# Kernel optimization log

Measured on AMD Instinct MI355X. Metric: run time of the kernel, lower is better.

## Reference

```python
import jax, jax.numpy as jnp
import numpy as np

N_LIG, N_PROT, K = 1024, 8192, 48
N = N_LIG + N_PROT
HID, FEAT, DEPTH = 256, 32, 5
NF = 6                      # sinusoid frequencies -> 12-dim distance embedding
EDGE_DIM = 4 * NF           # per-block dist emb (12) + top-level dist emb (12)
NORM = 5.0                  # agg_norm_factor
_FREQS = (2.0 * np.pi * 4.0 ** np.arange(NF) / 15.0).astype(np.float32)

def sin_emb(d2):
    # d2: [E,1] squared distances -> [E, 2*NF] sinusoidal embedding
    d = jnp.sqrt(d2 + 1e-8)
    x = d * _FREQS
    return jnp.concatenate([jnp.sin(x), jnp.cos(x)], axis=-1)

def knn_edges(coors):
    # KNN (k=48, no self loops) restricted to ligand query nodes (first N_LIG),
    # matching edges[:, :N_lig*k] slicing of knn_graph(flow='target_to_source').
    c = jax.lax.stop_gradient(coors)
    lig = c[:N_LIG]
    d2 = jnp.sum((lig[:, None, :] - c[None, :, :]) ** 2, axis=-1)  # [N_LIG, N]
    d2 = d2.at[jnp.arange(N_LIG), jnp.arange(N_LIG)].set(jnp.inf)
    _, idx = jax.lax.top_k(-d2, K)                                  # [N_LIG, K]
    row = jnp.repeat(jnp.arange(N_LIG), K)
    col = idx.reshape(-1)
    return row, col

def egnn(h, x, row, col, W_in, b_in, W_out, b_out, edge_W1, edge_b1, edge_W2, edge_b2, att_W, att_b, node_W1, node_b1, node_W2, node_b2, coord_W1, coord_b1, coord_W2, coord_b2, coord_W3):
    # EDM-style EGNN: per block 1 GCL (edge MLP + attention gate + node MLP residual)
    # followed by an equivariant coordinate update; sin distance embedding.
    emb0 = sin_emb(jnp.sum((x[row] - x[col]) ** 2, axis=-1, keepdims=True))
    h = h @ W_in + b_in
    for l in range(DEPTH):
        diff = x[row] - x[col]                         # [E,3]
        d2 = jnp.sum(diff ** 2, axis=-1, keepdims=True)
        cdiff = diff / (jnp.sqrt(d2 + 1e-8) + 1.0)     # norm_constant = 1
        ea = jnp.concatenate([sin_emb(d2), emb0], axis=-1)  # [E, EDGE_DIM]
        m = jax.nn.silu(jnp.concatenate([h[row], h[col], ea], axis=-1) @ edge_W1[l] + edge_b1[l])
        m = jax.nn.silu(m @ edge_W2[l] + edge_b2[l])
        m = m * jax.nn.sigmoid(m @ att_W[l] + att_b[l])         # attention gate
        agg = jax.ops.segment_sum(m, row, num_segments=N) / NORM
        u = jax.nn.silu(jnp.concatenate([h, agg], axis=-1) @ node_W1[l] + node_b1[l])
        h = h + (u @ node_W2[l] + node_b2[l])                    # residual node update
        c = jax.nn.silu(jnp.concatenate([h[row], h[col], ea], axis=-1) @ coord_W1[l] + coord_b1[l])  # use_latest_h
        c = jax.nn.silu(c @ coord_W2[l] + coord_b2[l])
        x = x + jax.ops.segment_sum(cdiff * (c @ coord_W3[l]), row, num_segments=N) / NORM
    return h @ W_out + b_out, x

def setup_inputs():
    key = jax.random.key(0)
    ks = jax.random.split(key, 24)
    f32 = jnp.float32
    def nrm(i, shape, scale=0.05):
        return jax.random.normal(ks[i], shape, dtype=f32) * scale
    return {
        'protein_positions': nrm(0, (N_PROT, 3), 3.0),
        'protein_ele': jax.random.randint(ks[1], (N_PROT,), 0, 5),
        'protein_amino_acid': jax.random.randint(ks[2], (N_PROT,), 0, 20),
        'protein_is_backbone': jax.random.randint(ks[3], (N_PROT,), 0, 2),
        'Xt_pos': nrm(4, (N_LIG, 3), 1.0),
        'Xt_features': nrm(5, (N_LIG, FEAT), 1.0),
        't': jax.random.randint(ks[6], (N_LIG,), 0, 1000),
        'Wt_time': nrm(7, (1000, 8), 1.0),
        'W_ele': nrm(8, (5, 16), 1.0),
        'W_aa': nrm(9, (20, 16), 1.0),
        'W_bb': nrm(10, (2, 8), 1.0),
        'W_in': nrm(11, (40, HID)), 'b_in': jnp.zeros((HID,), f32),
        'W_out': nrm(12, (HID, FEAT)), 'b_out': jnp.zeros((FEAT,), f32),
        'edge_W1': nrm(13, (DEPTH, 2 * HID + EDGE_DIM, HID)), 'edge_b1': jnp.zeros((DEPTH, HID), f32),
        'edge_W2': nrm(14, (DEPTH, HID, HID)), 'edge_b2': jnp.zeros((DEPTH, HID), f32),
        'att_W': nrm(15, (DEPTH, HID, 1)), 'att_b': jnp.zeros((DEPTH, 1), f32),
        'node_W1': nrm(16, (DEPTH, 2 * HID, HID)), 'node_b1': jnp.zeros((DEPTH, HID), f32),
        'node_W2': nrm(17, (DEPTH, HID, HID)), 'node_b2': jnp.zeros((DEPTH, HID), f32),
        'coord_W1': nrm(18, (DEPTH, 2 * HID + EDGE_DIM, HID)), 'coord_b1': jnp.zeros((DEPTH, HID), f32),
        'coord_W2': nrm(19, (DEPTH, HID, HID)), 'coord_b2': jnp.zeros((DEPTH, HID), f32),
        'coord_W3': nrm(20, (DEPTH, HID, 1), 0.001),
        'pos_w': jnp.ones((1, 1), f32),
    }

def reference(protein_positions, protein_ele, protein_amino_acid, protein_is_backbone, Xt_pos, Xt_features, t, Wt_time, W_ele, W_aa, W_bb, W_in, b_in, W_out, b_out, edge_W1, edge_b1, edge_W2, edge_b2, att_W, att_b, node_W1, node_b1, node_W2, node_b2, coord_W1, coord_b1, coord_W2, coord_b2, coord_W3, pos_w):
    prot_feat = jnp.concatenate([W_ele[protein_ele], W_aa[protein_amino_acid], W_bb[protein_is_backbone]], axis=-1)  # [N_PROT,40]
    feats = jnp.concatenate([jnp.concatenate([Xt_features, Wt_time[t]], axis=-1), prot_feat], axis=0)  # [N,40]
    coors = jnp.concatenate([Xt_pos, protein_positions], axis=0)  # [N,3]
    row, col = knn_edges(coors)
    h, x = egnn(feats, coors, row, col, W_in, b_in, W_out, b_out, edge_W1, edge_b1, edge_W2, edge_b2, att_W, att_b, node_W1, node_b1, node_W2, node_b2, coord_W1, coord_b1, coord_W2, coord_b2, coord_W3)
    # pos_linear: Linear(1,1,bias=False) applied elementwise == scalar multiply
    return x[:N_LIG] * pos_w[0, 0], h[:N_LIG]
```

## Files before the change

kernel.cpp:

```cpp
#include <hip/hip_runtime.h>
#include <hip/hip_bf16.h>
#include <math.h>

#define N_LIGC 1024
#define NTOT 9216
#define KNN 48
#define HID 256
#define DEPTHC 5
#define ETOT (N_LIGC*KNN)
#define KBINS 4096
#define PACK_BLKS 1484

typedef unsigned short u16;
typedef __attribute__((ext_vector_type(8))) short bf16x8;
typedef __attribute__((ext_vector_type(4))) float f32x4;

__device__ __forceinline__ float freq_f(int i){
  double p = (double)(1 << (2*i));
  return (float)((2.0*3.14159265358979323846)*p/15.0);
}
__device__ __forceinline__ float silu_f(float v){
  return v*__builtin_amdgcn_rcpf(1.0f+__expf(-v));
}
__device__ __forceinline__ float sigm_f(float v){
  return __builtin_amdgcn_rcpf(1.0f+__expf(-v));
}
__device__ __forceinline__ u16 f2b(float f){
  unsigned int u = __float_as_uint(f);
  return (u16)((u + 0x7fffu + ((u>>16)&1u)) >> 16);
}
__device__ __forceinline__ float b2f(u16 u){
  union { unsigned int i; float f; } c; c.i = ((unsigned int)u)<<16; return c.f;
}
__device__ __forceinline__ u16 f2b_p(float f){
  union { __hip_bfloat16 h; u16 u; } c; c.h = __float2bfloat16(f); return c.u;
}

__device__ __forceinline__ void pack_one(const float* __restrict__ src,
    u16* __restrict__ dst, int srcK, int kOff, int Keff, int Kp, int N, int idx)
{
  int lane = idx & 63;
  int rest = idx >> 6;
  int Nt = N >> 4;
  int n0 = rest % Nt;
  int rest2 = rest / Nt;
  int Kt = Kp >> 5;
  int k0 = rest2 % Kt;
  int layer = rest2 / Kt;
  int kq = lane >> 4, nl = lane & 15;
  int kb = k0*32 + kq*8, n = n0*16 + nl;
  u16 o[8];
  #pragma unroll
  for (int j=0;j<8;j++){
    int k = kb + j;
    float v = (k < Keff) ? src[((size_t)layer*srcK + kOff + k)*N + n] : 0.f;
    o[j] = f2b_p(v);
  }
  *(uint4*)(dst + (size_t)idx*8) = *(uint4*)o;
}

__global__ __launch_bounds__(256) void k_prep(
    const float* eW1, const float* eW2, const float* nW1, const float* nW2,
    const float* cW1, const float* cW2, const float* Wout,
    u16* eW1abP, u16* eW1cP, u16* eW2p, u16* nW1p, u16* nW2p,
    u16* cW1abP, u16* cW1cP, u16* cW2p, u16* WoutP,
    const float* __restrict__ protPos, const int* __restrict__ protEle,
    const int* __restrict__ protAA, const int* __restrict__ protBB,
    const float* __restrict__ XtPos, const float* __restrict__ XtFeat,
    const int* __restrict__ tArr, const float* __restrict__ WtTime,
    const float* __restrict__ Wele, const float* __restrict__ Waa,
    const float* __restrict__ Wbb,
    const float* __restrict__ Win, const float* __restrict__ bin,
    float* __restrict__ X0, float* __restrict__ X1,
    float* __restrict__ h, u16* __restrict__ h_bf)
{
  __shared__ float sF[8*40];
  if (blockIdx.x < PACK_BLKS){
    int idx = blockIdx.x*256 + threadIdx.x;
    if (idx < 81920){ pack_one(eW1, eW1abP, 536, 0,   512, 512, 256, idx); return; } idx -= 81920;
    if (idx < 5120 ){ pack_one(eW1, eW1cP,  536, 512, 24,  32,  256, idx); return; } idx -= 5120;
    if (idx < 40960){ pack_one(eW2, eW2p,   256, 0,   256, 256, 256, idx); return; } idx -= 40960;
    if (idx < 81920){ pack_one(nW1, nW1p,   512, 0,   512, 512, 256, idx); return; } idx -= 81920;
    if (idx < 40960){ pack_one(nW2, nW2p,   256, 0,   256, 256, 256, idx); return; } idx -= 40960;
    if (idx < 81920){ pack_one(cW1, cW1abP, 536, 0,   512, 512, 256, idx); return; } idx -= 81920;
    if (idx < 5120 ){ pack_one(cW1, cW1cP,  536, 512, 24,  32,  256, idx); return; } idx -= 5120;
    if (idx < 40960){ pack_one(cW2, cW2p,   256, 0,   256, 256, 256, idx); return; } idx -= 40960;
    if (idx < 1024 ){ pack_one(Wout, WoutP, 256, 0,   256, 256, 32,  idx); return; }
    return;
  }
  int blk=blockIdx.x - PACK_BLKS, tid=threadIdx.x;
  int n0=blk*8;
  for (int x=tid; x<344; x+=256){
    if (x < 320){
      int n = x/40, k = x%40;
      int node = n0+n;
      float v;
      if (node < N_LIGC){
        if (k < 32) v = XtFeat[node*32+k];
        else        v = WtTime[tArr[node]*8 + (k-32)];
      } else {
        int p = node - N_LIGC;
        if (k < 16)      v = Wele[protEle[p]*16 + k];
        else if (k < 32) v = Waa[protAA[p]*16 + (k-16)];
        else             v = Wbb[protBB[p]*8 + (k-32)];
      }
      sF[n*40+k] = v;
    } else {
      int r = x-320; int n = r/3, c = r%3;
      int node = n0+n;
      float v = (node < N_LIGC) ? XtPos[node*3+c] : protPos[(node-N_LIGC)*3+c];
      X0[node*3+c] = v; X1[node*3+c] = v;
    }
  }
  __syncthreads();
  float acc[8];
  float b=bin[tid];
  #pragma unroll
  for (int n=0;n<8;n++) acc[n]=b;
  for (int k=0;k<40;k++){
    float w=Win[k*HID+tid];
    #pragma unroll
    for (int n=0;n<8;n++) acc[n]+=sF[n*40+k]*w;
  }
  #pragma unroll
  for (int n=0;n<8;n++){
    h[(size_t)(n0+n)*HID+tid]=acc[n];
    h_bf[(size_t)(n0+n)*HID+tid]=f2b_p(acc[n]);
  }
}

__global__ __launch_bounds__(256) void k_knn(const float* __restrict__ X,
    int* __restrict__ col, u16* __restrict__ emb0)
{
  __shared__ unsigned int hist[KBINS];
  __shared__ unsigned int part[256];
  __shared__ float selD[KNN];
  __shared__ int   candI[512];
  __shared__ float candV[512];
  __shared__ int sB, sCless, sNeed, sNsel, sNcand;
  int b = blockIdx.x, tid = threadIdx.x;
  for (int i=tid;i<KBINS;i+=256) hist[i]=0u;
  if (tid==0){ sNsel=0; sNcand=0; }
  float px = X[b*3+0], py = X[b*3+1], pz = X[b*3+2];
  __syncthreads();
  #pragma unroll 4
  for (int j=0;j<36;j++){
    int i = tid + 256*j;
    float dx = __fsub_rn(px, X[i*3+0]);
    float dy = __fsub_rn(py, X[i*3+1]);
    float dz = __fsub_rn(pz, X[i*3+2]);
    float d2 = __fadd_rn(__fadd_rn(__fmul_rn(dx,dx),__fmul_rn(dy,dy)),__fmul_rn(dz,dz));
    if (i==b) d2 = INFINITY;
    unsigned key = __float_as_uint(d2) >> 19;
    atomicAdd(&hist[key], 1u);
  }
  __syncthreads();
  {
    unsigned s=0;
    #pragma unroll 4
    for (int k=0;k<16;k++) s += hist[tid*16+k];
    part[tid]=s;
  }
  __syncthreads();
  if (tid==0){
    unsigned c=0; int chunk=0;
    for (int t=0;t<256;t++){
      if (c + part[t] >= (unsigned)KNN){ chunk=t; break; }
      c += part[t];
    }
    int bin = chunk*16;
    for (;;bin++){
      unsigned hh = hist[bin];
      if (c + hh >= (unsigned)KNN) break;
      c += hh;
    }
    sB = bin; sCless = (int)c; sNeed = KNN - (int)c;
  }
  __syncthreads();
  int B = sB;
  #pragma unroll 4
  for (int j=0;j<36;j++){
    int i = tid + 256*j;
    float dx = __fsub_rn(px, X[i*3+0]);
    float dy = __fsub_rn(py, X[i*3+1]);
    float dz = __fsub_rn(pz, X[i*3+2]);
    float d2 = __fadd_rn(__fadd_rn(__fmul_rn(dx,dx),__fmul_rn(dy,dy)),__fmul_rn(dz,dz));
    if (i==b) d2 = INFINITY;
    int key = (int)(__float_as_uint(d2) >> 19);
    if (key < B){
      int p = atomicAdd(&sNsel, 1);
      col[b*KNN+p] = i; selD[p] = d2;
    } else if (key == B){
      int c = atomicAdd(&sNcand, 1);
      if (c < 512){ candI[c] = i; candV[c] = d2; }
    }
  }
  __syncthreads();
  if (tid < 64){
    int m = sNcand; if (m > 512) m = 512;
    int need = sNeed, base = sCless;
    float cv[8]; int ci[8];
    #pragma unroll
    for (int k=0;k<8;k++){
      int c = tid + 64*k;
      if (c < m){ ci[k]=candI[c]; cv[k]=candV[c]; }
      else      { ci[k]=0x7fffffff; cv[k]=INFINITY; }
    }
    for (int it=0; it<need; it++){
      float bv=INFINITY; int bi=0x7fffffff; int bk=0;
      #pragma unroll
      for (int k=0;k<8;k++){
        if (cv[k]<bv || (cv[k]==bv && ci[k]<bi)){ bv=cv[k]; bi=ci[k]; bk=k; }
      }
      int bslot = tid + 64*bk;
      #pragma unroll
      for (int off=32; off>=1; off>>=1){
        float ov = __shfl_down(bv, off);
        int   oi = __shfl_down(bi, off);
        int   os = __shfl_down(bslot, off);
        if (ov < bv || (ov==bv && oi<bi)){ bv=ov; bi=oi; bslot=os; }
      }
      int wslot = __shfl(bslot, 0);
      if (tid==0){ col[b*KNN+base+it]=bi; selD[base+it]=bv; }
      if ((wslot & 63) == tid) cv[wslot >> 6] = INFINITY;
    }
  }
  __syncthreads();
  if (tid < KNN){
    float d = sqrtf(selD[tid] + 1e-8f);
    int base = (b*KNN+tid)*12;
    #pragma unroll
    for (int i=0;i<6;i++){
      float fr = freq_f(i);
      emb0[base+i]   = f2b_p(sinf(d*fr));
      emb0[base+6+i] = f2b_p(cosf(d*fr));
    }
  }
}

__global__ __launch_bounds__(256) void k_pq(const u16* __restrict__ h_bf,
    const u16* __restrict__ Wab, float* __restrict__ R, u16* __restrict__ Qb, int l)
{
  __shared__ __align__(16) u16 sA[32*264];
  int blk=blockIdx.x, tid=threadIdx.x;
  int lane=tid&63, ng=tid>>6, quad=lane>>4, nl=lane&15;
  for (int t=tid; t<32*32; t+=256){
    int i=t>>5, q=t&31;
    uint4 v = ((const uint4*)(h_bf + (size_t)(blk*32+i)*HID))[q];
    *(uint4*)(sA + i*264 + q*8) = v;
  }
  __syncthreads();
  const u16* Wl = Wab + (size_t)l*512*HID;
  f32x4 zero4 = {0.f,0.f,0.f,0.f};
  f32x4 aQ[2][4];
  #pragma unroll
  for (int i=0;i<2;i++){ aQ[i][0]=zero4; aQ[i][1]=zero4; aQ[i][2]=zero4; aQ[i][3]=zero4; }
  #pragma unroll 2
  for (int k0=0;k0<8;k0++){
    bf16x8 a0 = *(const bf16x8*)(sA + (0*16+nl)*264 + k0*32 + quad*8);
    bf16x8 a1 = *(const bf16x8*)(sA + (1*16+nl)*264 + k0*32 + quad*8);
    const u16* wb = Wl + ((size_t)((k0+8)*16 + ng*4)*64 + lane)*8;
    bf16x8 b0 = *(const bf16x8*)(wb);
    bf16x8 b1 = *(const bf16x8*)(wb + 512);
    bf16x8 b2 = *(const bf16x8*)(wb + 1024);
    bf16x8 b3 = *(const bf16x8*)(wb + 1536);
    aQ[0][0]=__builtin_amdgcn_mfma_f32_16x16x32_bf16(a0,b0,aQ[0][0],0,0,0);
    aQ[0][1]=__builtin_amdgcn_mfma_f32_16x16x32_bf16(a0,b1,aQ[0][1],0,0,0);
    aQ[0][2]=__builtin_amdgcn_mfma_f32_16x16x32_bf16(a0,b2,aQ[0][2],0,0,0);
    aQ[0][3]=__builtin_amdgcn_mfma_f32_16x16x32_bf16(a0,b3,aQ[0][3],0,0,0);
    aQ[1][0]=__builtin_amdgcn_mfma_f32_16x16x32_bf16(a1,b0,aQ[1][0],0,0,0);
    aQ[1][1]=__builtin_amdgcn_mfma_f32_16x16x32_bf16(a1,b1,aQ[1][1],0,0,0);
    aQ[1][2]=__builtin_amdgcn_mfma_f32_16x16x32_bf16(a1,b2,aQ[1][2],0,0,0);
    aQ[1][3]=__builtin_amdgcn_mfma_f32_16x16x32_bf16(a1,b3,aQ[1][3],0,0,0);
  }
  #pragma unroll
  for (int mt=0;mt<2;mt++)
  #pragma unroll
  for (int nt=0;nt<4;nt++){
    int n = ng*64 + nt*16 + nl;
    #pragma unroll
    for (int r=0;r<4;r++){
      int node = blk*32 + mt*16 + quad*4 + r;
      Qb[(size_t)node*HID + n] = f2b(aQ[mt][nt][r]);
    }
  }
  if (blk < 32){
    f32x4 aR[2][4];
    #pragma unroll
    for (int i=0;i<2;i++){ aR[i][0]=zero4; aR[i][1]=zero4; aR[i][2]=zero4; aR[i][3]=zero4; }
    #pragma unroll 2
    for (int k0=0;k0<8;k0++){
      bf16x8 a0 = *(const bf16x8*)(sA + (0*16+nl)*264 + k0*32 + quad*8);
      bf16x8 a1 = *(const bf16x8*)(sA + (1*16+nl)*264 + k0*32 + quad*8);
      const u16* wb = Wl + ((size_t)(k0*16 + ng*4)*64 + lane)*8;
      bf16x8 b0 = *(const bf16x8*)(wb);
      bf16x8 b1 = *(const bf16x8*)(wb + 512);
      bf16x8 b2 = *(const bf16x8*)(wb + 1024);
      bf16x8 b3 = *(const bf16x8*)(wb + 1536);
      aR[0][0]=__builtin_amdgcn_mfma_f32_16x16x32_bf16(a0,b0,aR[0][0],0,0,0);
      aR[0][1]=__builtin_amdgcn_mfma_f32_16x16x32_bf16(a0,b1,aR[0][1],0,0,0);
      aR[0][2]=__builtin_amdgcn_mfma_f32_16x16x32_bf16(a0,b2,aR[0][2],0,0,0);
      aR[0][3]=__builtin_amdgcn_mfma_f32_16x16x32_bf16(a0,b3,aR[0][3],0,0,0);
      aR[1][0]=__builtin_amdgcn_mfma_f32_16x16x32_bf16(a1,b0,aR[1][0],0,0,0);
      aR[1][1]=__builtin_amdgcn_mfma_f32_16x16x32_bf16(a1,b1,aR[1][1],0,0,0);
      aR[1][2]=__builtin_amdgcn_mfma_f32_16x16x32_bf16(a1,b2,aR[1][2],0,0,0);
      aR[1][3]=__builtin_amdgcn_mfma_f32_16x16x32_bf16(a1,b3,aR[1][3],0,0,0);
    }
    #pragma unroll
    for (int mt=0;mt<2;mt++)
    #pragma unroll
    for (int nt=0;nt<4;nt++){
      int n = ng*64 + nt*16 + nl;
      #pragma unroll
      for (int r=0;r<4;r++){
        int node = blk*32 + mt*16 + quad*4 + r;
        R[(size_t)node*HID + n] = aR[mt][nt][r];
      }
    }
  }
}

__global__ __launch_bounds__(256,4) void k_comb_edge(
    const u16* __restrict__ Qb, const float* __restrict__ R,
    const float* __restrict__ xc,
    const int* __restrict__ colIdx, const u16* __restrict__ emb0,
    const u16* __restrict__ W1cP, const float* __restrict__ B1,
    const u16* __restrict__ W2p, const float* __restrict__ B2,
    const float* __restrict__ attW, const float* __restrict__ attB,
    u16* __restrict__ agg_bf, int l)
{
  __shared__ __align__(16) u16 sQ[48*264];
  __shared__ __align__(16) u16 sEA[48*40];
  __shared__ float sR[256];
  __shared__ int sCol[48];
  __shared__ float sD[48];
  __shared__ float sSig[48];
  __shared__ float sDot[48][4];

  int row = blockIdx.x, tid = threadIdx.x;
  int lane = tid & 63, ng = tid >> 6;
  int quad = lane >> 4, nl = lane & 15;

  if (tid < 48) sCol[tid] = colIdx[(size_t)row*KNN + tid];
  sR[tid] = R[(size_t)row*HID + tid];
  __syncthreads();
  for (int t = tid; t < 48*32; t += 256){
    int e = t >> 5, q = t & 31;
    uint4 v = ((const uint4*)(Qb + (size_t)sCol[e]*HID))[q];
    *(uint4*)(sQ + e*264 + q*8) = v;
  }
  if (tid < 48){
    int cg = sCol[tid];
    float dx = xc[row*3+0]-xc[cg*3+0];
    float dy = xc[row*3+1]-xc[cg*3+1];
    float dz = xc[row*3+2]-xc[cg*3+2];
    float d = sqrtf(dx*dx+dy*dy+dz*dz + 1e-8f);
    sD[tid] = d;
    const unsigned int* ep = (const unsigned int*)(emb0 + ((size_t)row*KNN + tid)*12);
    unsigned int* dd = (unsigned int*)(sEA + tid*40 + 12);
    #pragma unroll
    for (int i=0;i<6;i++) dd[i] = ep[i];
    u16* ea = sEA + tid*40;
    #pragma unroll
    for (int i=24;i<32;i++) ea[i] = 0;
  }
  __syncthreads();
  for (int t=tid; t<288; t+=256){
    int e = t/6, i = t - 6*e;
    float fr = 0.41887903f * (float)(1 << (2*i));
    float x = sD[e]*fr;
    u16* ea = sEA + e*40;
    ea[i]   = f2b(__sinf(x));
    ea[6+i] = f2b(__cosf(x));
  }
  __syncthreads();

  f32x4 zero4 = {0.f,0.f,0.f,0.f};
  f32x4 acc[3][4];
  #pragma unroll
  for (int i=0;i<3;i++){ acc[i][0]=zero4; acc[i][1]=zero4; acc[i][2]=zero4; acc[i][3]=zero4; }
  {
    const u16* Wc = W1cP + (size_t)l*32*HID;
    const u16* wb = Wc + ((size_t)(ng*4)*64 + lane)*8;
    bf16x8 b0 = *(const bf16x8*)(wb);
    bf16x8 b1 = *(const bf16x8*)(wb + 512);
    bf16x8 b2 = *(const bf16x8*)(wb + 1024);
    bf16x8 b3 = *(const bf16x8*)(wb + 1536);
    bf16x8 a0 = *(const bf16x8*)(sEA + (0*16+nl)*40 + quad*8);
    bf16x8 a1 = *(const bf16x8*)(sEA + (1*16+nl)*40 + quad*8);
    bf16x8 a2 = *(const bf16x8*)(sEA + (2*16+nl)*40 + quad*8);
    acc[0][0]=__builtin_amdgcn_mfma_f32_16x16x32_bf16(a0,b0,acc[0][0],0,0,0);
    acc[0][1]=__builtin_amdgcn_mfma_f32_16x16x32_bf16(a0,b1,acc[0][1],0,0,0);
    acc[0][2]=__builtin_amdgcn_mfma_f32_16x16x32_bf16(a0,b2,acc[0][2],0,0,0);
    acc[0][3]=__builtin_amdgcn_mfma_f32_16x16x32_bf16(a0,b3,acc[0][3],0,0,0);
    acc[1][0]=__builtin_amdgcn_mfma_f32_16x16x32_bf16(a1,b0,acc[1][0],0,0,0);
    acc[1][1]=__builtin_amdgcn_mfma_f32_16x16x32_bf16(a1,b1,acc[1][1],0,0,0);
    acc[1][2]=__builtin_amdgcn_mfma_f32_16x16x32_bf16(a1,b2,acc[1][2],0,0,0);
    acc[1][3]=__builtin_amdgcn_mfma_f32_16x16x32_bf16(a1,b3,acc[1][3],0,0,0);
    acc[2][0]=__builtin_amdgcn_mfma_f32_16x16x32_bf16(a2,b0,acc[2][0],0,0,0);
    acc[2][1]=__builtin_amdgcn_mfma_f32_16x16x32_bf16(a2,b1,acc[2][1],0,0,0);
    acc[2][2]=__builtin_amdgcn_mfma_f32_16x16x32_bf16(a2,b2,acc[2][2],0,0,0);
    acc[2][3]=__builtin_amdgcn_mfma_f32_16x16x32_bf16(a2,b3,acc[2][3],0,0,0);
  }
  #pragma unroll
  for (int mt=0;mt<3;mt++)
  #pragma unroll
  for (int nt=0;nt<4;nt++){
    int n = ng*64 + nt*16 + nl;
    float bb = B1[l*HID + n] + sR[n];
    #pragma unroll
    for (int r=0;r<4;r++){
      int m = mt*16 + quad*4 + r;
      float v = acc[mt][nt][r] + bb + b2f(sQ[m*264 + n]);
      sQ[m*264 + n] = f2b(silu_f(v));
    }
  }
  __syncthreads();

  f32x4 acc2[3][4];
  #pragma unroll
  for (int i=0;i<3;i++){ acc2[i][0]=zero4; acc2[i][1]=zero4; acc2[i][2]=zero4; acc2[i][3]=zero4; }
  const u16* W2 = W2p + (size_t)l*HID*HID;
  #pragma unroll 2
  for (int k0=0;k0<8;k0++){
    bf16x8 a0 = *(const bf16x8*)(sQ + (0*16+nl)*264 + k0*32 + quad*8);
    bf16x8 a1 = *(const bf16x8*)(sQ + (1*16+nl)*264 + k0*32 + quad*8);
    bf16x8 a2 = *(const bf16x8*)(sQ + (2*16+nl)*264 + k0*32 + quad*8);
    const u16* wb = W2 + ((size_t)(k0*16 + ng*4)*64 + lane)*8;
    bf16x8 b0 = *(const bf16x8*)(wb);
    bf16x8 b1 = *(const bf16x8*)(wb + 512);
    bf16x8 b2 = *(const bf16x8*)(wb + 1024);
    bf16x8 b3 = *(const bf16x8*)(wb + 1536);
    acc2[0][0]=__builtin_amdgcn_mfma_f32_16x16x32_bf16(a0,b0,acc2[0][0],0,0,0);
    acc2[0][1]=__builtin_amdgcn_mfma_f32_16x16x32_bf16(a0,b1,acc2[0][1],0,0,0);
    acc2[0][2]=__builtin_amdgcn_mfma_f32_16x16x32_bf16(a0,b2,acc2[0][2],0,0,0);
    acc2[0][3]=__builtin_amdgcn_mfma_f32_16x16x32_bf16(a0,b3,acc2[0][3],0,0,0);
    acc2[1][0]=__builtin_amdgcn_mfma_f32_16x16x32_bf16(a1,b0,acc2[1][0],0,0,0);
    acc2[1][1]=__builtin_amdgcn_mfma_f32_16x16x32_bf16(a1,b1,acc2[1][1],0,0,0);
    acc2[1][2]=__builtin_amdgcn_mfma_f32_16x16x32_bf16(a1,b2,acc2[1][2],0,0,0);
    acc2[1][3]=__builtin_amdgcn_mfma_f32_16x16x32_bf16(a1,b3,acc2[1][3],0,0,0);
    acc2[2][0]=__builtin_amdgcn_mfma_f32_16x16x32_bf16(a2,b0,acc2[2][0],0,0,0);
    acc2[2][1]=__builtin_amdgcn_mfma_f32_16x16x32_bf16(a2,b1,acc2[2][1],0,0,0);
    acc2[2][2]=__builtin_amdgcn_mfma_f32_16x16x32_bf16(a2,b2,acc2[2][2],0,0,0);
    acc2[2][3]=__builtin_amdgcn_mfma_f32_16x16x32_bf16(a2,b3,acc2[2][3],0,0,0);
  }
  float aw[4], bb2[4];
  #pragma unroll
  for (int nt=0;nt<4;nt++){
    int n = ng*64 + nt*16 + nl;
    aw[nt]  = attW[l*HID + n];
    bb2[nt] = B2[l*HID + n];
  }
  float dotp[3][4];
  #pragma unroll
  for (int mt=0;mt<3;mt++){
    #pragma unroll
    for (int r=0;r<4;r++) dotp[mt][r] = 0.f;
    #pragma unroll
    for (int nt=0;nt<4;nt++){
      #pragma unroll
      for (int r=0;r<4;r++){
        float s = silu_f(acc2[mt][nt][r] + bb2[nt]);
        acc2[mt][nt][r] = s;
        dotp[mt][r] += s*aw[nt];
      }
    }
  }
  #pragma unroll
  for (int off=1; off<16; off<<=1){
    #pragma unroll
    for (int mt=0;mt<3;mt++)
    #pragma unroll
    for (int r=0;r<4;r++)
      dotp[mt][r] += __shfl_xor(dotp[mt][r], off);
  }
  if (nl == 0){
    #pragma unroll
    for (int mt=0;mt<3;mt++)
    #pragma unroll
    for (int r=0;r<4;r++)
      sDot[mt*16 + quad*4 + r][ng] = dotp[mt][r];
  }
  __syncthreads();
  if (tid < 48) sSig[tid] = sigm_f(sDot[tid][0]+sDot[tid][1]+sDot[tid][2]+sDot[tid][3] + attB[l]);
  __syncthreads();
  float sgv[3][4];
  #pragma unroll
  for (int mt=0;mt<3;mt++)
  #pragma unroll
  for (int r=0;r<4;r++)
    sgv[mt][r] = sSig[mt*16 + quad*4 + r];
  #pragma unroll
  for (int nt=0;nt<4;nt++){
    float a = 0.f;
    #pragma unroll
    for (int mt=0;mt<3;mt++)
    #pragma unroll
    for (int r=0;r<4;r++)
      a += acc2[mt][nt][r]*sgv[mt][r];
    a += __shfl_xor(a, 16);
    a += __shfl_xor(a, 32);
    if (quad == 0) agg_bf[(size_t)row*HID + ng*64 + nt*16 + nl] = f2b(a*0.2f);
  }
}

__global__ __launch_bounds__(512,1) void k_node(
    float* __restrict__ h, u16* __restrict__ h_bf,
    const u16* __restrict__ agg_bf,
    const u16* __restrict__ W1p, const float* __restrict__ B1,
    const u16* __restrict__ W2p, const float* __restrict__ B2,
    const u16* __restrict__ cWab, u16* __restrict__ QbC, float* __restrict__ RC,
    const u16* __restrict__ eWabN, u16* __restrict__ QbE, float* __restrict__ RE, int doE,
    const u16* __restrict__ WoutP, const float* __restrict__ bout,
    float* __restrict__ outH, int doOut, int l)
{
  __shared__ __align__(16) u16 sA[48*520];
  __shared__ __align__(16) u16 sU[48*264];
  u16* sH = sA;
  int blk=blockIdx.x, tid=threadIdx.x;
  int lane=tid&63, wv=tid>>6, quad=lane>>4, nl=lane&15;
  int base = blk*36;
  for (int t=tid; t<48*64; t+=512){
    int i=t>>6, q=t&63;
    uint4 v;
    if (i < 36){
      int node = base+i;
      if (q<32) v = ((const uint4*)(h_bf + (size_t)node*HID))[q];
      else if (node < N_LIGC) v = ((const uint4*)(agg_bf + (size_t)node*HID))[q-32];
      else { v.x=0u; v.y=0u; v.z=0u; v.w=0u; }
    } else { v.x=0u; v.y=0u; v.z=0u; v.w=0u; }
    *(uint4*)(sA + i*520 + q*8) = v;
  }
  __syncthreads();
  f32x4 zero4 = {0.f,0.f,0.f,0.f};
  f32x4 acc[3][2];
  #pragma unroll
  for (int i=0;i<3;i++){ acc[i][0]=zero4; acc[i][1]=zero4; }
  const u16* Wp = W1p + (size_t)l*512*HID;
  #pragma unroll 2
  for (int k0=0;k0<16;k0++){
    bf16x8 a0 = *(const bf16x8*)(sA + (0*16+nl)*520 + k0*32 + quad*8);
    bf16x8 a1 = *(const bf16x8*)(sA + (1*16+nl)*520 + k0*32 + quad*8);
    bf16x8 a2 = *(const bf16x8*)(sA + (2*16+nl)*520 + k0*32 + quad*8);
    const u16* wb = Wp + ((size_t)(k0*16 + wv*2)*64 + lane)*8;
    bf16x8 b0 = *(const bf16x8*)(wb);
    bf16x8 b1 = *(const bf16x8*)(wb + 512);
    acc[0][0]=__builtin_amdgcn_mfma_f32_16x16x32_bf16(a0,b0,acc[0][0],0,0,0);
    acc[0][1]=__builtin_amdgcn_mfma_f32_16x16x32_bf16(a0,b1,acc[0][1],0,0,0);
    acc[1][0]=__builtin_amdgcn_mfma_f32_16x16x32_bf16(a1,b0,acc[1][0],0,0,0);
    acc[1][1]=__builtin_amdgcn_mfma_f32_16x16x32_bf16(a1,b1,acc[1][1],0,0,0);
    acc[2][0]=__builtin_amdgcn_mfma_f32_16x16x32_bf16(a2,b0,acc[2][0],0,0,0);
    acc[2][1]=__builtin_amdgcn_mfma_f32_16x16x32_bf16(a2,b1,acc[2][1],0,0,0);
  }
  #pragma unroll
  for (int mt=0;mt<3;mt++)
  #pragma unroll
  for (int nt=0;nt<2;nt++){
    int n = wv*32 + nt*16 + nl;
    float bb = B1[l*HID + n];
    #pragma unroll
    for (int r=0;r<4;r++){
      int m = mt*16 + quad*4 + r;
      sU[m*264 + n] = f2b(silu_f(acc[mt][nt][r] + bb));
    }
  }
  __syncthreads();
  f32x4 acc2[3][2];
  #pragma unroll
  for (int i=0;i<3;i++){ acc2[i][0]=zero4; acc2[i][1]=zero4; }
  const u16* W2 = W2p + (size_t)l*HID*HID;
  #pragma unroll 2
  for (int k0=0;k0<8;k0++){
    bf16x8 a0 = *(const bf16x8*)(sU + (0*16+nl)*264 + k0*32 + quad*8);
    bf16x8 a1 = *(const bf16x8*)(sU + (1*16+nl)*264 + k0*32 + quad*8);
    bf16x8 a2 = *(const bf16x8*)(sU + (2*16+nl)*264 + k0*32 + quad*8);
    const u16* wb = W2 + ((size_t)(k0*16 + wv*2)*64 + lane)*8;
    bf16x8 b0 = *(const bf16x8*)(wb);
    bf16x8 b1 = *(const bf16x8*)(wb + 512);
    acc2[0][0]=__builtin_amdgcn_mfma_f32_16x16x32_bf16(a0,b0,acc2[0][0],0,0,0);
    acc2[0][1]=__builtin_amdgcn_mfma_f32_16x16x32_bf16(a0,b1,acc2[0][1],0,0,0);
    acc2[1][0]=__builtin_amdgcn_mfma_f32_16x16x32_bf16(a1,b0,acc2[1][0],0,0,0);
    acc2[1][1]=__builtin_amdgcn_mfma_f32_16x16x32_bf16(a1,b1,acc2[1][1],0,0,0);
    acc2[2][0]=__builtin_amdgcn_mfma_f32_16x16x32_bf16(a2,b0,acc2[2][0],0,0,0);
    acc2[2][1]=__builtin_amdgcn_mfma_f32_16x16x32_bf16(a2,b1,acc2[2][1],0,0,0);
  }
  #pragma unroll
  for (int mt=0;mt<3;mt++)
  #pragma unroll
  for (int nt=0;nt<2;nt++){
    int n = wv*32 + nt*16 + nl;
    float bb = B2[l*HID + n];
    #pragma unroll
    for (int r=0;r<4;r++){
      int m = mt*16 + quad*4 + r;
      if (m < 36){
        size_t idx = (size_t)(base+m)*HID + n;
        float v = h[idx] + acc2[mt][nt][r] + bb;
        h[idx] = v;
        u16 bv = f2b(v);
        h_bf[idx] = bv;
        sH[m*264 + n] = bv;
      } else {
        sH[m*264 + n] = 0;
      }
    }
  }
  __syncthreads();

  int isLig = (base < N_LIGC);
  const u16* Wl = cWab + (size_t)l*512*HID;
  f32x4 q[3][2];
  #pragma unroll
  for (int i=0;i<3;i++){ q[i][0]=zero4; q[i][1]=zero4; }
  #pragma unroll 2
  for (int k0=0;k0<8;k0++){
    bf16x8 a0 = *(const bf16x8*)(sH + (0*16+nl)*264 + k0*32 + quad*8);
    bf16x8 a1 = *(const bf16x8*)(sH + (1*16+nl)*264 + k0*32 + quad*8);
    bf16x8 a2 = *(const bf16x8*)(sH + (2*16+nl)*264 + k0*32 + quad*8);
    const u16* wb = Wl + ((size_t)((k0+8)*16 + wv*2)*64 + lane)*8;
// ... 75 lines not shown
      for (int r=0;r<4;r++){
        int m = mt*16 + quad*4 + r;
        if (m < 36) QbE[(size_t)(base+m)*HID + n] = f2b(q[mt][nt][r]);
      }
    }
    if (isLig){
      #pragma unroll
      for (int i=0;i<3;i++){ q[i][0]=zero4; q[i][1]=zero4; }
      #pragma unroll 2
      for (int k0=0;k0<8;k0++){
        bf16x8 a0 = *(const bf16x8*)(sH + (0*16+nl)*264 + k0*32 + quad*8);
        bf16x8 a1 = *(const bf16x8*)(sH + (1*16+nl)*264 + k0*32 + quad*8);
        bf16x8 a2 = *(const bf16x8*)(sH + (2*16+nl)*264 + k0*32 + quad*8);
        const u16* wb = eWabN + ((size_t)(k0*16 + wv*2)*64 + lane)*8;
        bf16x8 b0 = *(const bf16x8*)(wb);
        bf16x8 b1 = *(const bf16x8*)(wb + 512);
        q[0][0]=__builtin_amdgcn_mfma_f32_16x16x32_bf16(a0,b0,q[0][0],0,0,0);
        q[0][1]=__builtin_amdgcn_mfma_f32_16x16x32_bf16(a0,b1,q[0][1],0,0,0);
        q[1][0]=__builtin_amdgcn_mfma_f32_16x16x32_bf16(a1,b0,q[1][0],0,0,0);
        q[1][1]=__builtin_amdgcn_mfma_f32_16x16x32_bf16(a1,b1,q[1][1],0,0,0);
        q[2][0]=__builtin_amdgcn_mfma_f32_16x16x32_bf16(a2,b0,q[2][0],0,0,0);
        q[2][1]=__builtin_amdgcn_mfma_f32_16x16x32_bf16(a2,b1,q[2][1],0,0,0);
      }
      #pragma unroll
      for (int mt=0;mt<3;mt++)
      #pragma unroll
      for (int nt=0;nt<2;nt++){
        int n = wv*32 + nt*16 + nl;
        #pragma unroll
        for (int r=0;r<4;r++){
          int m = mt*16 + quad*4 + r;
          int node = base + m;
          if (m < 36 && node < N_LIGC) RE[(size_t)node*HID + n] = q[mt][nt][r];
        }
      }
    }
  }
  if (doOut && isLig && wv < 2){
    int ntw = wv;
    f32x4 o[3]; o[0]=zero4; o[1]=zero4; o[2]=zero4;
    #pragma unroll 2
    for (int k0=0;k0<8;k0++){
      bf16x8 b = *(const bf16x8*)(WoutP + ((size_t)(k0*2 + ntw)*64 + lane)*8);
      #pragma unroll
      for (int mt=0;mt<3;mt++){
        bf16x8 a = *(const bf16x8*)(sH + (mt*16+nl)*264 + k0*32 + quad*8);
        o[mt] = __builtin_amdgcn_mfma_f32_16x16x32_bf16(a,b,o[mt],0,0,0);
      }
    }
    int n = ntw*16 + nl;
    float bb = bout[n];
    #pragma unroll
    for (int mt=0;mt<3;mt++)
    #pragma unroll
    for (int r=0;r<4;r++){
      int m = mt*16 + quad*4 + r;
      int node = base + m;
      if (m < 36 && node < N_LIGC)
        outH[(size_t)node*32 + n] = o[mt][r] + bb;
    }
  }
}

__global__ __launch_bounds__(256,4) void k_comb_coord(
    const u16* __restrict__ Qb, const float* __restrict__ R,
    const float* __restrict__ xc, float* __restrict__ xn,
    const int* __restrict__ colIdx, const u16* __restrict__ emb0,
    const u16* __restrict__ W1cP, const float* __restrict__ B1,
    const u16* __restrict__ W2p, const float* __restrict__ B2,
    const float* __restrict__ cW3,
    const float* __restrict__ posw, float* __restrict__ outX, int doOut, int l)
{
  __shared__ __align__(16) u16 sQ[48*264];
  __shared__ __align__(16) u16 sEA[48*40];
  __shared__ float sR[256];
  __shared__ int sCol[48];
  __shared__ float sD[48];
  __shared__ float sCd[48*3];
  __shared__ float sS[48];
  __shared__ float sDot[48][4];

  int row = blockIdx.x, tid = threadIdx.x;
  int lane = tid & 63, ng = tid >> 6;
  int quad = lane >> 4, nl = lane & 15;

  if (tid < 48) sCol[tid] = colIdx[(size_t)row*KNN + tid];
  sR[tid] = R[(size_t)row*HID + tid];
  __syncthreads();
  for (int t = tid; t < 48*32; t += 256){
    int e = t >> 5, q = t & 31;
    uint4 v = ((const uint4*)(Qb + (size_t)sCol[e]*HID))[q];
    *(uint4*)(sQ + e*264 + q*8) = v;
  }
  if (tid < 48){
    int cg = sCol[tid];
    float dx = xc[row*3+0]-xc[cg*3+0];
    float dy = xc[row*3+1]-xc[cg*3+1];
    float dz = xc[row*3+2]-xc[cg*3+2];
    float d = sqrtf(dx*dx+dy*dy+dz*dz + 1e-8f);
    sD[tid] = d;
    float rden = __builtin_amdgcn_rcpf(d + 1.0f);
    sCd[tid*3+0]=dx*rden; sCd[tid*3+1]=dy*rden; sCd[tid*3+2]=dz*rden;
    const unsigned int* ep = (const unsigned int*)(emb0 + ((size_t)row*KNN + tid)*12);
    unsigned int* dd = (unsigned int*)(sEA + tid*40 + 12);
    #pragma unroll
    for (int i=0;i<6;i++) dd[i] = ep[i];
    u16* ea = sEA + tid*40;
    #pragma unroll
    for (int i=24;i<32;i++) ea[i] = 0;
  }
  __syncthreads();
  for (int t=tid; t<288; t+=256){
    int e = t/6, i = t - 6*e;
    float fr = 0.41887903f * (float)(1 << (2*i));
    float x = sD[e]*fr;
    u16* ea = sEA + e*40;
    ea[i]   = f2b(__sinf(x));
    ea[6+i] = f2b(__cosf(x));
  }
  __syncthreads();

  f32x4 zero4 = {0.f,0.f,0.f,0.f};
  f32x4 acc[3][4];
  #pragma unroll
  for (int i=0;i<3;i++){ acc[i][0]=zero4; acc[i][1]=zero4; acc[i][2]=zero4; acc[i][3]=zero4; }
  {
    const u16* Wc = W1cP + (size_t)l*32*HID;
    const u16* wb = Wc + ((size_t)(ng*4)*64 + lane)*8;
    bf16x8 b0 = *(const bf16x8*)(wb);
    bf16x8 b1 = *(const bf16x8*)(wb + 512);
    bf16x8 b2 = *(const bf16x8*)(wb + 1024);
    bf16x8 b3 = *(const bf16x8*)(wb + 1536);
    bf16x8 a0 = *(const bf16x8*)(sEA + (0*16+nl)*40 + quad*8);
    bf16x8 a1 = *(const bf16x8*)(sEA + (1*16+nl)*40 + quad*8);
    bf16x8 a2 = *(const bf16x8*)(sEA + (2*16+nl)*40 + quad*8);
    acc[0][0]=__builtin_amdgcn_mfma_f32_16x16x32_bf16(a0,b0,acc[0][0],0,0,0);
    acc[0][1]=__builtin_amdgcn_mfma_f32_16x16x32_bf16(a0,b1,acc[0][1],0,0,0);
    acc[0][2]=__builtin_amdgcn_mfma_f32_16x16x32_bf16(a0,b2,acc[0][2],0,0,0);
    acc[0][3]=__builtin_amdgcn_mfma_f32_16x16x32_bf16(a0,b3,acc[0][3],0,0,0);
    acc[1][0]=__builtin_amdgcn_mfma_f32_16x16x32_bf16(a1,b0,acc[1][0],0,0,0);
    acc[1][1]=__builtin_amdgcn_mfma_f32_16x16x32_bf16(a1,b1,acc[1][1],0,0,0);
    acc[1][2]=__builtin_amdgcn_mfma_f32_16x16x32_bf16(a1,b2,acc[1][2],0,0,0);
    acc[1][3]=__builtin_amdgcn_mfma_f32_16x16x32_bf16(a1,b3,acc[1][3],0,0,0);
    acc[2][0]=__builtin_amdgcn_mfma_f32_16x16x32_bf16(a2,b0,acc[2][0],0,0,0);
    acc[2][1]=__builtin_amdgcn_mfma_f32_16x16x32_bf16(a2,b1,acc[2][1],0,0,0);
    acc[2][2]=__builtin_amdgcn_mfma_f32_16x16x32_bf16(a2,b2,acc[2][2],0,0,0);
    acc[2][3]=__builtin_amdgcn_mfma_f32_16x16x32_bf16(a2,b3,acc[2][3],0,0,0);
  }
  #pragma unroll
  for (int mt=0;mt<3;mt++)
  #pragma unroll
  for (int nt=0;nt<4;nt++){
    int n = ng*64 + nt*16 + nl;
    float bb = B1[l*HID + n] + sR[n];
    #pragma unroll
    for (int r=0;r<4;r++){
      int m = mt*16 + quad*4 + r;
      float v = acc[mt][nt][r] + bb + b2f(sQ[m*264 + n]);
      sQ[m*264 + n] = f2b(silu_f(v));
    }
  }
  __syncthreads();

  f32x4 acc2[3][4];
  #pragma unroll
  for (int i=0;i<3;i++){ acc2[i][0]=zero4; acc2[i][1]=zero4; acc2[i][2]=zero4; acc2[i][3]=zero4; }
  const u16* W2 = W2p + (size_t)l*HID*HID;
  #pragma unroll 2
  for (int k0=0;k0<8;k0++){
    bf16x8 a0 = *(const bf16x8*)(sQ + (0*16+nl)*264 + k0*32 + quad*8);
    bf16x8 a1 = *(const bf16x8*)(sQ + (1*16+nl)*264 + k0*32 + quad*8);
    bf16x8 a2 = *(const bf16x8*)(sQ + (2*16+nl)*264 + k0*32 + quad*8);
    const u16* wb = W2 + ((size_t)(k0*16 + ng*4)*64 + lane)*8;
    bf16x8 b0 = *(const bf16x8*)(wb);
    bf16x8 b1 = *(const bf16x8*)(wb + 512);
    bf16x8 b2 = *(const bf16x8*)(wb + 1024);
    bf16x8 b3 = *(const bf16x8*)(wb + 1536);
    acc2[0][0]=__builtin_amdgcn_mfma_f32_16x16x32_bf16(a0,b0,acc2[0][0],0,0,0);
    acc2[0][1]=__builtin_amdgcn_mfma_f32_16x16x32_bf16(a0,b1,acc2[0][1],0,0,0);
    acc2[0][2]=__builtin_amdgcn_mfma_f32_16x16x32_bf16(a0,b2,acc2[0][2],0,0,0);
    acc2[0][3]=__builtin_amdgcn_mfma_f32_16x16x32_bf16(a0,b3,acc2[0][3],0,0,0);
    acc2[1][0]=__builtin_amdgcn_mfma_f32_16x16x32_bf16(a1,b0,acc2[1][0],0,0,0);
    acc2[1][1]=__builtin_amdgcn_mfma_f32_16x16x32_bf16(a1,b1,acc2[1][1],0,0,0);
    acc2[1][2]=__builtin_amdgcn_mfma_f32_16x16x32_bf16(a1,b2,acc2[1][2],0,0,0);
    acc2[1][3]=__builtin_amdgcn_mfma_f32_16x16x32_bf16(a1,b3,acc2[1][3],0,0,0);
    acc2[2][0]=__builtin_amdgcn_mfma_f32_16x16x32_bf16(a2,b0,acc2[2][0],0,0,0);
    acc2[2][1]=__builtin_amdgcn_mfma_f32_16x16x32_bf16(a2,b1,acc2[2][1],0,0,0);
    acc2[2][2]=__builtin_amdgcn_mfma_f32_16x16x32_bf16(a2,b2,acc2[2][2],0,0,0);
    acc2[2][3]=__builtin_amdgcn_mfma_f32_16x16x32_bf16(a2,b3,acc2[2][3],0,0,0);
  }
  float cw[4], bb2[4];
  #pragma unroll
  for (int nt=0;nt<4;nt++){
    int n = ng*64 + nt*16 + nl;
    cw[nt]  = cW3[l*HID + n];
    bb2[nt] = B2[l*HID + n];
  }
  float dotp[3][4];
  #pragma unroll
  for (int mt=0;mt<3;mt++){
    #pragma unroll
    for (int r=0;r<4;r++) dotp[mt][r] = 0.f;
    #pragma unroll
    for (int nt=0;nt<4;nt++){
      #pragma unroll
      for (int r=0;r<4;r++){
        float s = silu_f(acc2[mt][nt][r] + bb2[nt]);
        dotp[mt][r] += s*cw[nt];
      }
    }
  }
  #pragma unroll
  for (int off=1; off<16; off<<=1){
    #pragma unroll
    for (int mt=0;mt<3;mt++)
    #pragma unroll
    for (int r=0;r<4;r++)
      dotp[mt][r] += __shfl_xor(dotp[mt][r], off);
  }
  if (nl == 0){
    #pragma unroll
    for (int mt=0;mt<3;mt++)
    #pragma unroll
    for (int r=0;r<4;r++)
      sDot[mt*16 + quad*4 + r][ng] = dotp[mt][r];
  }
  __syncthreads();
  if (tid < 48) sS[tid] = sDot[tid][0]+sDot[tid][1]+sDot[tid][2]+sDot[tid][3];
  __syncthreads();
  if (tid < 3){
    float u = 0.f;
    #pragma unroll 4
    for (int e=0;e<48;e++) u += sCd[e*3+tid]*sS[e];
    float nv = xc[row*3+tid] + u*0.2f;
    xn[row*3+tid] = nv;
    if (doOut) outX[row*3+tid] = nv*posw[0];
  }
}

extern "C" void kernel_launch(void* const* d_in, const int* in_sizes, int n_in,
                              void* d_out, int out_size, void* d_ws, size_t ws_size,
                              hipStream_t stream)
{
  const float* protPos = (const float*)d_in[0];
  const int*   protEle = (const int*)d_in[1];
  const int*   protAA  = (const int*)d_in[2];
  const int*   protBB  = (const int*)d_in[3];
  const float* XtPos   = (const float*)d_in[4];
  const float* XtFeat  = (const float*)d_in[5];
  const int*   tArr    = (const int*)d_in[6];
  const float* WtTime  = (const float*)d_in[7];
  const float* Wele    = (const float*)d_in[8];
  const float* Waa     = (const float*)d_in[9];
  const float* Wbb     = (const float*)d_in[10];
  const float* Win     = (const float*)d_in[11];
  const float* bin     = (const float*)d_in[12];
  const float* Wout    = (const float*)d_in[13];
  const float* bout    = (const float*)d_in[14];
  const float* eW1     = (const float*)d_in[15];
  const float* eB1     = (const float*)d_in[16];
  const float* eW2     = (const float*)d_in[17];
  const float* eB2     = (const float*)d_in[18];
  const float* attW    = (const float*)d_in[19];
  const float* attB    = (const float*)d_in[20];
  const float* nW1     = (const float*)d_in[21];
  const float* nB1     = (const float*)d_in[22];
  const float* nW2     = (const float*)d_in[23];
  const float* nB2     = (const float*)d_in[24];
  const float* cW1     = (const float*)d_in[25];
  const float* cB1     = (const float*)d_in[26];
  const float* cW2     = (const float*)d_in[27];
  const float* cB2     = (const float*)d_in[28];
  const float* cW3     = (const float*)d_in[29];
  const float* posw    = (const float*)d_in[30];

  float* fp = (float*)d_ws;
  float* X0   = fp;               fp += NTOT*3;
  float* X1   = fp;               fp += NTOT*3;
  float* h    = fp;               fp += (size_t)NTOT*HID;
  float* RC   = fp;               fp += (size_t)N_LIGC*HID;
  float* RE   = fp;               fp += (size_t)N_LIGC*HID;
  int*   col  = (int*)fp;         fp += ETOT;
  u16*   up   = (u16*)fp;
  u16* emb0   = up;               up += (size_t)ETOT*12;
  u16* h_bf   = up;               up += (size_t)NTOT*HID;
  u16* agg_bf = up;               up += (size_t)N_LIGC*HID;
  u16* QbE    = up;               up += (size_t)NTOT*HID;
  u16* QbC    = up;               up += (size_t)NTOT*HID;
  u16* eW1abP = up;               up += (size_t)DEPTHC*512*HID;
  u16* eW1cP  = up;               up += (size_t)DEPTHC*32*HID;
  u16* eW2p   = up;               up += (size_t)DEPTHC*HID*HID;
  u16* nW1p   = up;               up += (size_t)DEPTHC*512*HID;
  u16* nW2p   = up;               up += (size_t)DEPTHC*HID*HID;
  u16* cW1abP = up;               up += (size_t)DEPTHC*512*HID;
  u16* cW1cP  = up;               up += (size_t)DEPTHC*32*HID;
  u16* cW2p   = up;               up += (size_t)DEPTHC*HID*HID;
  u16* WoutP  = up;               up += (size_t)256*32;

  k_prep<<<PACK_BLKS + NTOT/8,256,0,stream>>>(eW1,eW2,nW1,nW2,cW1,cW2,Wout,
      eW1abP,eW1cP,eW2p,nW1p,nW2p,cW1abP,cW1cP,cW2p,WoutP,
      protPos,protEle,protAA,protBB,XtPos,XtFeat,
      tArr,WtTime,Wele,Waa,Wbb,Win,bin,X0,X1,h,h_bf);
  k_knn<<<N_LIGC,256,0,stream>>>(X0,col,emb0);
  k_pq<<<NTOT/32,256,0,stream>>>(h_bf,eW1abP,RE,QbE,0);

  float* xc = X0; float* xn = X1;
  float* outF = (float*)d_out;
  for (int l=0;l<DEPTHC;l++){
    k_comb_edge<<<N_LIGC,256,0,stream>>>(QbE,RE,xc,col,emb0,eW1cP,eB1,eW2p,eB2,attW,attB,agg_bf,l);
    const u16* eNext = eW1abP + (size_t)((l+1)%DEPTHC)*512*HID;
    k_node<<<256,512,0,stream>>>(h,h_bf,agg_bf,nW1p,nB1,nW2p,nB2,
        cW1abP,QbC,RC, eNext,QbE,RE,(l<DEPTHC-1)?1:0,
        WoutP,bout, outF+3072, (l==DEPTHC-1)?1:0, l);
    k_comb_coord<<<N_LIGC,256,0,stream>>>(QbC,RC,xc,xn,col,emb0,cW1cP,cB1,cW2p,cB2,cW3,
        posw, outF, (l==DEPTHC-1)?1:0, l);
    float* t2=xc; xc=xn; xn=t2;
  }
}
```

Baseline: 503.5 us.

## Cache KNN distances in registers, parallel scan threshold, retile k_pq to 256 blocks

In the KNN kernel, squared distances are kept in a 36-entry register array so the second pass no longer reloads coordinates and recomputes them. The serial single-thread chunk search is replaced by a block-wide parallel prefix scan. k_pq is retiled to 256 blocks of 512 threads, each handling 36 nodes padded to 48 rows, so the grid maps one block per CU. The padding adds wasted MFMA work and the register array raises register pressure in k_knn.

```diff
diff --git a/kernel.cpp b/kernel.cpp
--- a/kernel.cpp
+++ b/kernel.cpp
@@ -133,17 +133,18 @@
     int* __restrict__ col, u16* __restrict__ emb0)
 {
   __shared__ unsigned int hist[KBINS];
-  __shared__ unsigned int part[256];
+  __shared__ unsigned int scanb[256];
   __shared__ float selD[KNN];
   __shared__ int   candI[512];
   __shared__ float candV[512];
-  __shared__ int sB, sCless, sNeed, sNsel, sNcand;
+  __shared__ int sB, sCless, sNeed, sNsel, sNcand, sChunk, sCbase;
   int b = blockIdx.x, tid = threadIdx.x;
   for (int i=tid;i<KBINS;i+=256) hist[i]=0u;
   if (tid==0){ sNsel=0; sNcand=0; }
   float px = X[b*3+0], py = X[b*3+1], pz = X[b*3+2];
   __syncthreads();
-  #pragma unroll 4
+  float d2v[36];
+  #pragma unroll
   for (int j=0;j<36;j++){
     int i = tid + 256*j;
     float dx = __fsub_rn(px, X[i*3+0]);
@@ -151,24 +152,33 @@
     float dz = __fsub_rn(pz, X[i*3+2]);
     float d2 = __fadd_rn(__fadd_rn(__fmul_rn(dx,dx),__fmul_rn(dy,dy)),__fmul_rn(dz,dz));
     if (i==b) d2 = INFINITY;
+    d2v[j] = d2;
     unsigned key = __float_as_uint(d2) >> 19;
     atomicAdd(&hist[key], 1u);
   }
   __syncthreads();
+  unsigned s=0;
   {
-    unsigned s=0;
     #pragma unroll 4
     for (int k=0;k<16;k++) s += hist[tid*16+k];
-    part[tid]=s;
+    scanb[tid]=s;
+  }
+  __syncthreads();
+  #pragma unroll
+  for (int off=1; off<256; off<<=1){
+    unsigned v = (tid>=off) ? scanb[tid-off] : 0u;
+    __syncthreads();
+    scanb[tid] += v;
+    __syncthreads();
+  }
+  {
+    unsigned incl = scanb[tid];
+    unsigned excl = incl - s;
+    if (excl < (unsigned)KNN && incl >= (unsigned)KNN){ sChunk = tid; sCbase = (int)excl; }
   }
   __syncthreads();
   if (tid==0){
-    unsigned c=0; int chunk=0;
-    for (int t=0;t<256;t++){
-      if (c + part[t] >= (unsigned)KNN){ chunk=t; break; }
-      c += part[t];
-    }
-    int bin = chunk*16;
+    unsigned c = (unsigned)sCbase; int bin = sChunk*16;
     for (;;bin++){
       unsigned hh = hist[bin];
       if (c + hh >= (unsigned)KNN) break;
@@ -178,14 +188,10 @@
   }
   __syncthreads();
   int B = sB;
-  #pragma unroll 4
+  #pragma unroll
   for (int j=0;j<36;j++){
     int i = tid + 256*j;
-    float dx = __fsub_rn(px, X[i*3+0]);
-    float dy = __fsub_rn(py, X[i*3+1]);
-    float dz = __fsub_rn(pz, X[i*3+2]);
-    float d2 = __fadd_rn(__fadd_rn(__fmul_rn(dx,dx),__fmul_rn(dy,dy)),__fmul_rn(dz,dz));
-    if (i==b) d2 = INFINITY;
+    float d2 = d2v[j];
     int key = (int)(__float_as_uint(d2) >> 19);
     if (key < B){
       int p = atomicAdd(&sNsel, 1);
@@ -238,83 +244,81 @@
   }
 }
 
-__global__ __launch_bounds__(256) void k_pq(const u16* __restrict__ h_bf,
+__global__ __launch_bounds__(512,1) void k_pq(const u16* __restrict__ h_bf,
     const u16* __restrict__ Wab, float* __restrict__ R, u16* __restrict__ Qb, int l)
 {
-  __shared__ __align__(16) u16 sA[32*264];
+  __shared__ __align__(16) u16 sA[48*264];
   int blk=blockIdx.x, tid=threadIdx.x;
-  int lane=tid&63, ng=tid>>6, quad=lane>>4, nl=lane&15;
-  for (int t=tid; t<32*32; t+=256){
+  int lane=tid&63, wv=tid>>6, quad=lane>>4, nl=lane&15;
+  int base = blk*36;
+  for (int t=tid; t<48*32; t+=512){
     int i=t>>5, q=t&31;
-    uint4 v = ((const uint4*)(h_bf + (size_t)(blk*32+i)*HID))[q];
+    uint4 v;
+    if (i < 36) v = ((const uint4*)(h_bf + (size_t)(base+i)*HID))[q];
+    else { v.x=0u; v.y=0u; v.z=0u; v.w=0u; }
     *(uint4*)(sA + i*264 + q*8) = v;
   }
   __syncthreads();
   const u16* Wl = Wab + (size_t)l*512*HID;
   f32x4 zero4 = {0.f,0.f,0.f,0.f};
-  f32x4 aQ[2][4];
-  #pragma unroll
-  for (int i=0;i<2;i++){ aQ[i][0]=zero4; aQ[i][1]=zero4; aQ[i][2]=zero4; aQ[i][3]=zero4; }
+  f32x4 aQ[3][2];
+  #pragma unroll
+  for (int i=0;i<3;i++){ aQ[i][0]=zero4; aQ[i][1]=zero4; }
   #pragma unroll 2
   for (int k0=0;k0<8;k0++){
     bf16x8 a0 = *(const bf16x8*)(sA + (0*16+nl)*264 + k0*32 + quad*8);
     bf16x8 a1 = *(const bf16x8*)(sA + (1*16+nl)*264 + k0*32 + quad*8);
-    const u16* wb = Wl + ((size_t)((k0+8)*16 + ng*4)*64 + lane)*8;
+    bf16x8 a2 = *(const bf16x8*)(sA + (2*16+nl)*264 + k0*32 + quad*8);
+    const u16* wb = Wl + ((size_t)((k0+8)*16 + wv*2)*64 + lane)*8;
     bf16x8 b0 = *(const bf16x8*)(wb);
     bf16x8 b1 = *(const bf16x8*)(wb + 512);
-    bf16x8 b2 = *(const bf16x8*)(wb + 1024);
-    bf16x8 b3 = *(const bf16x8*)(wb + 1536);
     aQ[0][0]=__builtin_amdgcn_mfma_f32_16x16x32_bf16(a0,b0,aQ[0][0],0,0,0);
     aQ[0][1]=__builtin_amdgcn_mfma_f32_16x16x32_bf16(a0,b1,aQ[0][1],0,0,0);
-    aQ[0][2]=__builtin_amdgcn_mfma_f32_16x16x32_bf16(a0,b2,aQ[0][2],0,0,0);
-    aQ[0][3]=__builtin_amdgcn_mfma_f32_16x16x32_bf16(a0,b3,aQ[0][3],0,0,0);
     aQ[1][0]=__builtin_amdgcn_mfma_f32_16x16x32_bf16(a1,b0,aQ[1][0],0,0,0);
     aQ[1][1]=__builtin_amdgcn_mfma_f32_16x16x32_bf16(a1,b1,aQ[1][1],0,0,0);
-    aQ[1][2]=__builtin_amdgcn_mfma_f32_16x16x32_bf16(a1,b2,aQ[1][2],0,0,0);
-    aQ[1][3]=__builtin_amdgcn_mfma_f32_16x16x32_bf16(a1,b3,aQ[1][3],0,0,0);
-  }
-  #pragma unroll
-  for (int mt=0;mt<2;mt++)
-  #pragma unroll
-  for (int nt=0;nt<4;nt++){
-    int n = ng*64 + nt*16 + nl;
+    aQ[2][0]=__builtin_amdgcn_mfma_f32_16x16x32_bf16(a2,b0,aQ[2][0],0,0,0);
+    aQ[2][1]=__builtin_amdgcn_mfma_f32_16x16x32_bf16(a2,b1,aQ[2][1],0,0,0);
+  }
+  #pragma unroll
+  for (int mt=0;mt<3;mt++)
+  #pragma unroll
+  for (int nt=0;nt<2;nt++){
+    int n = wv*32 + nt*16 + nl;
     #pragma unroll
     for (int r=0;r<4;r++){
-      int node = blk*32 + mt*16 + quad*4 + r;
-      Qb[(size_t)node*HID + n] = f2b(aQ[mt][nt][r]);
-    }
-  }
-  if (blk < 32){
-    f32x4 aR[2][4];
-    #pragma unroll
-    for (int i=0;i<2;i++){ aR[i][0]=zero4; aR[i][1]=zero4; aR[i][2]=zero4; aR[i][3]=zero4; }
+      int m = mt*16 + quad*4 + r;
+      if (m < 36) Qb[(size_t)(base+m)*HID + n] = f2b(aQ[mt][nt][r]);
+    }
+  }
+  if (base < N_LIGC){
+    f32x4 aR[3][2];
+    #pragma unroll
+    for (int i=0;i<3;i++){ aR[i][0]=zero4; aR[i][1]=zero4; }
     #pragma unroll 2
     for (int k0=0;k0<8;k0++){
       bf16x8 a0 = *(const bf16x8*)(sA + (0*16+nl)*264 + k0*32 + quad*8);
       bf16x8 a1 = *(const bf16x8*)(sA + (1*16+nl)*264 + k0*32 + quad*8);
-      const u16* wb = Wl + ((size_t)(k0*16 + ng*4)*64 + lane)*8;
+      bf16x8 a2 = *(const bf16x8*)(sA + (2*16+nl)*264 + k0*32 + quad*8);
+      const u16* wb = Wl + ((size_t)(k0*16 + wv*2)*64 + lane)*8;
       bf16x8 b0 = *(const bf16x8*)(wb);
       bf16x8 b1 = *(const bf16x8*)(wb + 512);
-      bf16x8 b2 = *(const bf16x8*)(wb + 1024);
-      bf16x8 b3 = *(const bf16x8*)(wb + 1536);
       aR[0][0]=__builtin_amdgcn_mfma_f32_16x16x32_bf16(a0,b0,aR[0][0],0,0,0);
       aR[0][1]=__builtin_amdgcn_mfma_f32_16x16x32_bf16(a0,b1,aR[0][1],0,0,0);
-      aR[0][2]=__builtin_amdgcn_mfma_f32_16x16x32_bf16(a0,b2,aR[0][2],0,0,0);
-      aR[0][3]=__builtin_amdgcn_mfma_f32_16x16x32_bf16(a0,b3,aR[0][3],0,0,0);
       aR[1][0]=__builtin_amdgcn_mfma_f32_16x16x32_bf16(a1,b0,aR[1][0],0,0,0);
       aR[1][1]=__builtin_amdgcn_mfma_f32_16x16x32_bf16(a1,b1,aR[1][1],0,0,0);
-      aR[1][2]=__builtin_amdgcn_mfma_f32_16x16x32_bf16(a1,b2,aR[1][2],0,0,0);
-      aR[1][3]=__builtin_amdgcn_mfma_f32_16x16x32_bf16(a1,b3,aR[1][3],0,0,0);
-    }
-    #pragma unroll
-    for (int mt=0;mt<2;mt++)
-    #pragma unroll
-    for (int nt=0;nt<4;nt++){
-      int n = ng*64 + nt*16 + nl;
+      aR[2][0]=__builtin_amdgcn_mfma_f32_16x16x32_bf16(a2,b0,aR[2][0],0,0,0);
+      aR[2][1]=__builtin_amdgcn_mfma_f32_16x16x32_bf16(a2,b1,aR[2][1],0,0,0);
+    }
+    #pragma unroll
+    for (int mt=0;mt<3;mt++)
+    #pragma unroll
+    for (int nt=0;nt<2;nt++){
+      int n = wv*32 + nt*16 + nl;
       #pragma unroll
       for (int r=0;r<4;r++){
-        int node = blk*32 + mt*16 + quad*4 + r;
-        R[(size_t)node*HID + n] = aR[mt][nt][r];
+        int m = mt*16 + quad*4 + r;
+        int node = base + m;
+        if (m < 36 && node < N_LIGC) R[(size_t)node*HID + n] = aR[mt][nt][r];
       }
     }
   }
@@ -996,7 +1000,7 @@
       protPos,protEle,protAA,protBB,XtPos,XtFeat,
       tArr,WtTime,Wele,Waa,Wbb,Win,bin,X0,X1,h,h_bf);
   k_knn<<<N_LIGC,256,0,stream>>>(X0,col,emb0);
-  k_pq<<<NTOT/32,256,0,stream>>>(h_bf,eW1abP,RE,QbE,0);
+  k_pq<<<256,512,0,stream>>>(h_bf,eW1abP,RE,QbE,0);
 
   float* xc = X0; float* xn = X1;
   float* outF = (float*)d_out;
```

Result: no change. 500.0 us (-0.7%).
